# Performance work log

Hardware: AMD Instinct MI355X
Metric: run time of the kernel (lower is better)

The kernel has to match this reference:

```python
import jax, jax.numpy as jnp
import numpy as np

N = 100000   # atoms
E = 1600000  # edges (unused by this readout but required by signature)
C = 128      # channel multiplicity of node_feats irreps 128x0e+128x1o
PATH_W = 1.0 / 16.0  # e3nn uvu path weight: sqrt(1/(mul2_path0 + mul2_path1)) = sqrt(1/256)
SQRT3 = float(np.sqrt(3.0))


def setup_inputs() -> dict:
    key = jax.random.key(0)
    ks = jax.random.split(key, 32)
    r = lambda k, s, sc=1.0: jax.random.normal(k, s, dtype=jnp.float32) * sc
    z = lambda s: jnp.zeros(s, dtype=jnp.float32)
    return {
        # forward args
        "node_attrs": r(ks[0], (N, 10)),
        "node_feats": r(ks[1], (N, 4 * C)),           # 128x0e (128) + 128x1o (384)
        "edge_attrs": r(ks[2], (E, 9)),
        "edge_feats": r(ks[3], (E, 8)),
        "edge_index": jax.random.randint(ks[4], (2, E), 0, N),
        "field_feats": r(ks[5], (N, 4)),               # 1x0e + 1x1o
        "charges_0": r(ks[6], (N, 1)),
        "charges_induced": r(ks[7], (N, 1)),
        # o3.Linear(charges_irreps -> node_feats_irreps), fan_in=1 -> plain weight
        "Wq0": r(ks[8], (1, C)), "bq": z((C,)),
        # o3.Linear(potential_irreps -> node_feats_irreps)
        "Wv0": r(ks[9], (1, C)), "bv": z((C,)),
        "Wv1": r(ks[10], (1, C)),                      # 1o -> 128x1o path (no bias)
        # SparseUvuTensorProduct weights: path0 (0e x 0e -> 0e), path1 (1o x 1o -> 0e)
        "wq_s": r(ks[11], (C, C)), "wq_v": r(ks[12], (C, C)),
        "wv_s": r(ks[13], (C, C)), "wv_v": r(ks[14], (C, C)),
        # readout MLP [256,128,128,128,1] with SiLU between layers
        "W1": r(ks[15], (2 * C, 128), 1.0 / np.sqrt(2 * C)), "b1": z((128,)),
        "W2": r(ks[16], (128, 128), 1.0 / np.sqrt(128)), "b2": z((128,)),
        "W3": r(ks[17], (128, 128), 1.0 / np.sqrt(128)), "b3": z((128,)),
        "W4": r(ks[18], (128, 1), 1.0 / np.sqrt(128)), "b4": z((1,)),
    }


def _sparse_uvu_tp(x1s, x1v, x2s, x2v, w_s, w_v):
    """uvu TP (128x0e+128x1o) x (128x0e+128x1o) -> 128x0e, both paths to i_out=0.
    x1s/x2s: [N,C], x1v/x2v: [N,C,3]. Avoids the [N,C,C] pair matrix by
    contracting the weight into x2 first."""
    # path 0e x 0e -> 0e (d=1): mixed_bu = x1_bu * sum_v x2_bv w_uv
    out = x1s * (x2s @ w_s.T)
    # path 1o x 1o -> 0e (d=3): mixed_bu = sum_{v,d} x1_bud x2_bvd w_uv / sqrt(3)
    t = jnp.einsum('bvd,uv->bud', x2v, w_v)
    out = out + jnp.sum(x1v * t, axis=-1) / SQRT3
    return PATH_W * out


def reference(node_attrs, node_feats, edge_attrs, edge_feats, edge_index,
              field_feats, charges_0, charges_induced,
              Wq0, bq, Wv0, bv, Wv1,
              wq_s, wq_v, wv_s, wv_v,
              W1, b1, W2, b2, W3, b3, W4, b4):
    n = node_feats.shape[0]
    node_s = node_feats[:, :C]                 # [N,128] scalar block
    node_v = node_feats[:, C:].reshape(n, C, 3)  # [N,128,3] vector block (mul_ir)

    # q branch: linear_up_q(charges_induced + charges_0)
    q_in = charges_induced + charges_0         # [N,1]
    q_up_s = q_in @ Wq0 + bq                   # [N,128]
    q_up_v = jnp.zeros((n, C, 3), node_feats.dtype)  # 1x0e has no path to 128x1o

    # v branch: linear_up_v(field_feats)
    v_up_s = field_feats[:, :1] @ Wv0 + bv                     # [N,128]
    v_up_v = field_feats[:, None, 1:4] * Wv1[0][None, :, None]  # [N,128,3]

    dot_q = _sparse_uvu_tp(node_s, node_v, q_up_s, q_up_v, wq_s, wq_v)  # [N,128]
    dot_v = _sparse_uvu_tp(node_s, node_v, v_up_s, v_up_v, wv_s, wv_v)  # [N,128]

    h = jnp.concatenate([dot_q, dot_v], axis=-1)  # [N,256]
    h = jax.nn.silu(h @ W1 + b1)
    h = jax.nn.silu(h @ W2 + b2)
    h = jax.nn.silu(h @ W3 + b3)
    return h @ W4 + b4                           # [N,1] per-atom energy readout
```

## Files before the change

kernel.cpp:

```cpp
#include <hip/hip_runtime.h>
#include <hip/hip_bf16.h>

typedef __attribute__((ext_vector_type(8))) short short8;
typedef __attribute__((ext_vector_type(4))) float f32x4;

#define PATH_W 0.0625f
#define INV_SQRT3 0.57735026918962576f

typedef const __attribute__((address_space(1))) char gchar;
typedef __attribute__((address_space(3))) char schar;

__device__ __forceinline__ unsigned short f2bf(float f) {
    unsigned int u = __builtin_bit_cast(unsigned int, f);
    u += 0x7FFFu + ((u >> 16) & 1u);
    return (unsigned short)(u >> 16);
}

__device__ __forceinline__ float silu(float x) {
    return x / (1.0f + __expf(-x));
}

__global__ void prep_all(const float* __restrict__ Wq0, const float* __restrict__ bq,
                         const float* __restrict__ Wv0, const float* __restrict__ bv,
                         const float* __restrict__ Wv1, const float* __restrict__ wq_s,
                         const float* __restrict__ wv_s, const float* __restrict__ wv_v,
                         const float* __restrict__ W1, const float* __restrict__ W2,
                         const float* __restrict__ W3, const float* __restrict__ b1,
                         const float* __restrict__ b2, const float* __restrict__ b3,
                         const float* __restrict__ W4, const float* __restrict__ b4,
                         float* __restrict__ vecs, unsigned short* __restrict__ wp) {
    if (blockIdx.x == 0) {
        int u = threadIdx.x;
        float aq = 0.f, bqs = 0.f, av = 0.f, bvs = 0.f, a1 = 0.f;
        for (int v = 0; v < 128; ++v) {
            float rq = wq_s[u * 128 + v];
            float rv = wv_s[u * 128 + v];
            aq  += Wq0[v] * rq;
            bqs += bq[v]  * rq;
            av  += Wv0[v] * rv;
            bvs += bv[v]  * rv;
            a1  += Wv1[v] * wv_v[u * 128 + v];
        }
        vecs[u]        = PATH_W * aq;
        vecs[128 + u]  = PATH_W * bqs;
        vecs[256 + u]  = PATH_W * av;
        vecs[384 + u]  = PATH_W * bvs;
        vecs[512 + u]  = PATH_W * INV_SQRT3 * a1;
        vecs[640 + u]  = b1[u];
        vecs[768 + u]  = b2[u];
        vecs[896 + u]  = b3[u];
        vecs[1024 + u] = W4[u];
        if (u == 0) { vecs[1152] = b4[0]; vecs[1153] = 0.f; vecs[1154] = 0.f; vecs[1155] = 0.f; }
        return;
    }
    int fid  = blockIdx.x - 1;
    int t    = threadIdx.x;
    int lane = t & 63;
    int half = t >> 6;
    int g  = lane >> 4;
    int r  = lane & 15;
    const float* W;
    int row0, col;
    if (fid < 64) {
        int mt = fid >> 3, ks = fid & 7;
        W = W1; col = mt * 16 + r;
        row0 = ks * 32 + g * 8 + half * 4;
    } else {
        int f2 = fid < 96 ? fid - 64 : fid - 96;
        int mt = f2 >> 2, ks = f2 & 3;
        W = fid < 96 ? W2 : W3; col = mt * 16 + r;
        row0 = half * 64 + ks * 16 + g * 4;
    }
    unsigned short* dst = wp + fid * 512 + lane * 8 + half * 4;
    #pragma unroll
    for (int j = 0; j < 4; ++j) dst[j] = f2bf(W[(row0 + j) * 128 + col]);
}

__global__ __launch_bounds__(512, 1) void fused_main(
    const float* __restrict__ nf,
    const float* __restrict__ field,
    const float* __restrict__ c0, const float* __restrict__ ci,
    const float* __restrict__ vecs,
    const unsigned short* __restrict__ wp,
    float* __restrict__ out, int N)
{
    __shared__ __align__(16) char smem[131072];
    __shared__ __align__(16) float vlds[1156];
    const int tid  = threadIdx.x;
    const int wave = tid >> 6;
    const int lane = tid & 63;
    const int g    = lane >> 4;
    const int nl   = lane & 15;
    const int T    = (N + 127) >> 7;
    const char* wpb = (const char*)wp;

    #pragma unroll
    for (int i = 0; i < 16; ++i) {
        int off = (wave * 16 + i) * 1024;
        __builtin_amdgcn_global_load_lds((gchar*)(wpb + off + lane * 16),
                                         (schar*)(smem + off), 16, 0, 0);
    }
    if (wave == 0) {
        #pragma unroll
        for (int i = 0; i < 5; ++i) {
            int idx = lane + 64 * i;
            if (idx < 289)
                reinterpret_cast<f32x4*>(vlds)[idx] =
                    reinterpret_cast<const f32x4*>(vecs)[idx];
        }
    }

    f32x4 hs[4], hv0[4], hv1[4], hv2[4];
    float c0r, cir; f32x4 ffr;
    const char* bsr; const char* bvr;

#define SLOT_LOAD(sl_, q_, h_, bs_, bv_) {                                    \
        hs[sl_]  = *reinterpret_cast<const f32x4*>((bs_) + 128 * (q_) + 16 * (h_)); \
        hv0[sl_] = *reinterpret_cast<const f32x4*>((bv_) + 384 * (q_) + 48 * (h_)); \
        hv1[sl_] = *reinterpret_cast<const f32x4*>((bv_) + 384 * (q_) + 48 * (h_) + 16); \
        hv2[sl_] = *reinterpret_cast<const f32x4*>((bv_) + 384 * (q_) + 48 * (h_) + 32); }

    int tile = blockIdx.x;
    {
        int nd0 = tile * 128 + wave * 16 + nl;
        int ndc = nd0 < N ? nd0 : N - 1;
        const char* nrow = (const char*)nf + (size_t)ndc * 2048;
        bsr = nrow + 32 * g;
        bvr = nrow + 512 + 96 * g;
        #pragma unroll
        for (int qh = 0; qh < 2; ++qh)
            #pragma unroll
            for (int h = 0; h < 2; ++h)
                SLOT_LOAD(2 * qh + h, qh, h, bsr, bvr)
        c0r = c0[ndc]; cir = ci[ndc];
        ffr = reinterpret_cast<const f32x4*>(field)[ndc];
    }

    __syncthreads();

    const f32x4* vl4 = reinterpret_cast<const f32x4*>(vlds);

    for (; tile < T; tile += gridDim.x) {
        const int nd = tile * 128 + wave * 16 + nl;
        const int nt = tile + gridDim.x;
        const bool hasnext = nt < T;

        const char* bsn = bsr; const char* bvn = bvr;
        float c0n = 0.f, cin = 0.f; f32x4 ffn = ffr;
        if (hasnext) {
            int ndn = nt * 128 + wave * 16 + nl;
            ndn = ndn < N ? ndn : N - 1;
            const char* nrow = (const char*)nf + (size_t)ndn * 2048;
            bsn = nrow + 32 * g;
            bvn = nrow + 512 + 96 * g;
            c0n = c0[ndn]; cin = ci[ndn];
            ffn = reinterpret_cast<const f32x4*>(field)[ndn];
        }

        const float q_in = c0r + cir;
        const f32x4 ff   = ffr;

        f32x4 acc[8];
        #pragma unroll
        for (int mt = 0; mt < 8; ++mt) acc[mt] = vl4[160 + mt * 4 + g];

        short8 hfA, hfB;
        #pragma unroll
        for (int half = 0; half < 2; ++half) {
            #pragma unroll
            for (int qh = 0; qh < 2; ++qh) {
                const int q = 2 * half + qh;
                #pragma unroll
                for (int h = 0; h < 2; ++h) {
                    const int slot = 2 * qh + h;
                    const int m = 8 * q + 2 * g + h;
                    f32x4 aq = vl4[m], bqv = vl4[32 + m], av = vl4[64 + m],
                          bvv = vl4[96 + m], a1 = vl4[128 + m];
                    f32x4 s = hs[slot], va = hv0[slot], vb = hv1[slot], vc = hv2[slot];
                    float d3[4];
                    d3[0] = fmaf(va[0], ff[1], fmaf(va[1], ff[2], va[2] * ff[3]));
                    d3[1] = fmaf(va[3], ff[1], fmaf(vb[0], ff[2], vb[1] * ff[3]));
                    d3[2] = fmaf(vb[2], ff[1], fmaf(vb[3], ff[2], vc[0] * ff[3]));
                    d3[3] = fmaf(vc[1], ff[1], fmaf(vc[2], ff[2], vc[3] * ff[3]));
                    #pragma unroll
                    for (int j = 0; j < 4; ++j) {
                        float hq = s[j] * fmaf(q_in, aq[j], bqv[j]);
                        float hv = fmaf(s[j], fmaf(ff[0], av[j], bvv[j]), a1[j] * d3[j]);
                        if (h == 0) { hfA[j]     = (short)f2bf(hq); hfB[j]     = (short)f2bf(hv); }
                        else        { hfA[4 + j] = (short)f2bf(hq); hfB[4 + j] = (short)f2bf(hv); }
                    }
                    __builtin_amdgcn_sched_barrier(0);
                    if (half == 0) {
                        SLOT_LOAD(slot, qh + 2, h, bsr, bvr)
                    } else if (hasnext) {
                        SLOT_LOAD(slot, qh, h, bsn, bvn)
                    }
                }
                #pragma unroll
                for (int mt = 0; mt < 8; ++mt) {
                    short8 a0 = *reinterpret_cast<const short8*>(
                        smem + (mt * 8 + q) * 1024 + lane * 16);
                    acc[mt] = __builtin_amdgcn_mfma_f32_16x16x32_bf16(a0, hfA, acc[mt], 0, 0, 0);
                    short8 a4 = *reinterpret_cast<const short8*>(
                        smem + (mt * 8 + q + 4) * 1024 + lane * 16);
                    acc[mt] = __builtin_amdgcn_mfma_f32_16x16x32_bf16(a4, hfB, acc[mt], 0, 0, 0);
                }
            }
        }

        short8 hf2[4];
        #pragma unroll
        for (int ks = 0; ks < 4; ++ks)
            #pragma unroll
            for (int hp = 0; hp < 2; ++hp)
                #pragma unroll
                for (int j = 0; j < 4; ++j)
                    hf2[ks][hp * 4 + j] = (short)f2bf(silu(acc[hp * 4 + ks][j]));

        f32x4 acc2[8];
        #pragma unroll
        for (int mt = 0; mt < 8; ++mt) acc2[mt] = vl4[192 + mt * 4 + g];
        #pragma unroll
        for (int ks = 0; ks < 4; ++ks) {
            #pragma unroll
            for (int mt = 0; mt < 8; ++mt) {
                short8 a = *reinterpret_cast<const short8*>(
                    smem + 65536 + (mt * 4 + ks) * 1024 + lane * 16);
                acc2[mt] = __builtin_amdgcn_mfma_f32_16x16x32_bf16(a, hf2[ks], acc2[mt], 0, 0, 0);
            }
        }

        short8 hf3[4];
        #pragma unroll
        for (int ks = 0; ks < 4; ++ks)
            #pragma unroll
            for (int hp = 0; hp < 2; ++hp)
                #pragma unroll
                for (int j = 0; j < 4; ++j)
                    hf3[ks][hp * 4 + j] = (short)f2bf(silu(acc2[hp * 4 + ks][j]));

        f32x4 acc3[8];
        #pragma unroll
        for (int mt = 0; mt < 8; ++mt) acc3[mt] = vl4[224 + mt * 4 + g];
        #pragma unroll
        for (int ks = 0; ks < 4; ++ks) {
            #pragma unroll
            for (int mt = 0; mt < 8; ++mt) {
                short8 a = *reinterpret_cast<const short8*>(
                    smem + 98304 + (mt * 4 + ks) * 1024 + lane * 16);
                acc3[mt] = __builtin_amdgcn_mfma_f32_16x16x32_bf16(a, hf3[ks], acc3[mt], 0, 0, 0);
            }
        }

        float acc_out = 0.f;
        #pragma unroll
        for (int mt = 0; mt < 8; ++mt) {
            f32x4 w4v = vl4[256 + mt * 4 + g];
            acc_out += silu(acc3[mt][0]) * w4v[0];
            acc_out += silu(acc3[mt][1]) * w4v[1];
            acc_out += silu(acc3[mt][2]) * w4v[2];
            acc_out += silu(acc3[mt][3]) * w4v[3];
        }
        acc_out += __shfl_xor(acc_out, 16, 64);
        acc_out += __shfl_xor(acc_out, 32, 64);
        if (g == 0 && nd < N) out[nd] = acc_out + vlds[1152];

        bsr = bsn; bvr = bvn;
        c0r = c0n; cir = cin; ffr = ffn;
    }
#undef SLOT_LOAD
}

extern "C" void kernel_launch(void* const* d_in, const int* in_sizes, int n_in,
                              void* d_out, int out_size, void* d_ws, size_t ws_size,
                              hipStream_t stream) {
    const float* node_feats = (const float*)d_in[1];
    const float* field      = (const float*)d_in[5];
    const float* c0         = (const float*)d_in[6];
    const float* ci         = (const float*)d_in[7];
    const float* Wq0        = (const float*)d_in[8];
    const float* bq         = (const float*)d_in[9];
    const float* Wv0        = (const float*)d_in[10];
    const float* bv         = (const float*)d_in[11];
    const float* Wv1        = (const float*)d_in[12];
    const float* wq_s       = (const float*)d_in[13];
    const float* wv_s       = (const float*)d_in[15];
    const float* wv_v       = (const float*)d_in[16];
    const float* W1         = (const float*)d_in[17];
    const float* b1         = (const float*)d_in[18];
    const float* W2         = (const float*)d_in[19];
    const float* b2         = (const float*)d_in[20];
    const float* W3         = (const float*)d_in[21];
    const float* b3         = (const float*)d_in[22];
    const float* W4         = (const float*)d_in[23];
    const float* b4         = (const float*)d_in[24];

    const int N = in_sizes[1] / 512;
    float* vecs = (float*)d_ws;
    unsigned short* wp = (unsigned short*)((char*)d_ws + 8192);

    prep_all<<<129, 128, 0, stream>>>(Wq0, bq, Wv0, bv, Wv1, wq_s, wv_s, wv_v,
                                      W1, W2, W3, b1, b2, b3, W4, b4, vecs, wp);
    const int T = (N + 127) / 128;
    const int blocks = T < 256 ? T : 256;
    fused_main<<<blocks, 512, 0, stream>>>(node_feats, field, c0, ci, vecs, wp,
                                           (float*)d_out, N);
}
```

Before: 73.98 us.

## Run two 8-wave sub-blocks per 1024-thread block sharing LDS weights

Doubles the block to 1024 threads, split into two independent 8-wave groups that each stride over their own 128-node tiles, while the packed bf16 weights in LDS are loaded once and shared. The register prefetch of node features shrinks from four slots to a two-slot rolling buffer, and the launch bounds change to allow more waves per SIMD. The aim is more resident waves per CU to hide global-load latency in this memory-heavy readout. The tighter register budget risks spills, and each slot now has less prefetch lead time.

```diff
diff --git a/kernel.cpp b/kernel.cpp
--- a/kernel.cpp
+++ b/kernel.cpp
@@ -76,7 +76,7 @@
     for (int j = 0; j < 4; ++j) dst[j] = f2bf(W[(row0 + j) * 128 + col]);
 }
 
-__global__ __launch_bounds__(512, 1) void fused_main(
+__global__ __launch_bounds__(1024, 4) void fused_main(
     const float* __restrict__ nf,
     const float* __restrict__ field,
     const float* __restrict__ c0, const float* __restrict__ ci,
@@ -89,14 +89,17 @@
     const int tid  = threadIdx.x;
     const int wave = tid >> 6;
     const int lane = tid & 63;
+    const int sb   = wave >> 3;
+    const int w8   = wave & 7;
     const int g    = lane >> 4;
     const int nl   = lane & 15;
     const int T    = (N + 127) >> 7;
+    const int stride = gridDim.x * 2;
     const char* wpb = (const char*)wp;
 
     #pragma unroll
-    for (int i = 0; i < 16; ++i) {
-        int off = (wave * 16 + i) * 1024;
+    for (int i = 0; i < 8; ++i) {
+        int off = (wave * 8 + i) * 1024;
         __builtin_amdgcn_global_load_lds((gchar*)(wpb + off + lane * 16),
                                          (schar*)(smem + off), 16, 0, 0);
     }
@@ -110,7 +113,7 @@
         }
     }
 
-    f32x4 hs[4], hv0[4], hv1[4], hv2[4];
+    f32x4 hs[2], hv0[2], hv1[2], hv2[2];
     float c0r, cir; f32x4 ffr;
     const char* bsr; const char* bvr;
 
@@ -120,35 +123,32 @@
         hv1[sl_] = *reinterpret_cast<const f32x4*>((bv_) + 384 * (q_) + 48 * (h_) + 16); \
         hv2[sl_] = *reinterpret_cast<const f32x4*>((bv_) + 384 * (q_) + 48 * (h_) + 32); }
 
-    int tile = blockIdx.x;
+    int tile = blockIdx.x * 2 + sb;
     {
-        int nd0 = tile * 128 + wave * 16 + nl;
+        int nd0 = tile * 128 + w8 * 16 + nl;
         int ndc = nd0 < N ? nd0 : N - 1;
         const char* nrow = (const char*)nf + (size_t)ndc * 2048;
         bsr = nrow + 32 * g;
         bvr = nrow + 512 + 96 * g;
-        #pragma unroll
-        for (int qh = 0; qh < 2; ++qh)
-            #pragma unroll
-            for (int h = 0; h < 2; ++h)
-                SLOT_LOAD(2 * qh + h, qh, h, bsr, bvr)
         c0r = c0[ndc]; cir = ci[ndc];
         ffr = reinterpret_cast<const f32x4*>(field)[ndc];
+        SLOT_LOAD(0, 0, 0, bsr, bvr)
+        SLOT_LOAD(1, 0, 1, bsr, bvr)
     }
 
     __syncthreads();
 
     const f32x4* vl4 = reinterpret_cast<const f32x4*>(vlds);
 
-    for (; tile < T; tile += gridDim.x) {
-        const int nd = tile * 128 + wave * 16 + nl;
-        const int nt = tile + gridDim.x;
+    for (; tile < T; tile += stride) {
+        const int nd = tile * 128 + w8 * 16 + nl;
+        const int nt = tile + stride;
         const bool hasnext = nt < T;
 
         const char* bsn = bsr; const char* bvn = bvr;
         float c0n = 0.f, cin = 0.f; f32x4 ffn = ffr;
         if (hasnext) {
-            int ndn = nt * 128 + wave * 16 + nl;
+            int ndn = nt * 128 + w8 * 16 + nl;
             ndn = ndn < N ? ndn : N - 1;
             const char* nrow = (const char*)nf + (size_t)ndn * 2048;
             bsn = nrow + 32 * g;
@@ -166,45 +166,43 @@
 
         short8 hfA, hfB;
         #pragma unroll
-        for (int half = 0; half < 2; ++half) {
-            #pragma unroll
-            for (int qh = 0; qh < 2; ++qh) {
-                const int q = 2 * half + qh;
+        for (int q = 0; q < 4; ++q) {
+            #pragma unroll
+            for (int h = 0; h < 2; ++h) {
+                const int p = 2 * q + h;
+                const int slot = p & 1;
+                const int m = 8 * q + 2 * g + h;
+                f32x4 aq = vl4[m], bqv = vl4[32 + m], av = vl4[64 + m],
+                      bvv = vl4[96 + m], a1 = vl4[128 + m];
+                f32x4 s = hs[slot], va = hv0[slot], vb = hv1[slot], vc = hv2[slot];
+                float d3[4];
+                d3[0] = fmaf(va[0], ff[1], fmaf(va[1], ff[2], va[2] * ff[3]));
+                d3[1] = fmaf(va[3], ff[1], fmaf(vb[0], ff[2], vb[1] * ff[3]));
+                d3[2] = fmaf(vb[2], ff[1], fmaf(vb[3], ff[2], vc[0] * ff[3]));
+                d3[3] = fmaf(vc[1], ff[1], fmaf(vc[2], ff[2], vc[3] * ff[3]));
                 #pragma unroll
-                for (int h = 0; h < 2; ++h) {
-                    const int slot = 2 * qh + h;
-                    const int m = 8 * q + 2 * g + h;
-                    f32x4 aq = vl4[m], bqv = vl4[32 + m], av = vl4[64 + m],
-                          bvv = vl4[96 + m], a1 = vl4[128 + m];
-                    f32x4 s = hs[slot], va = hv0[slot], vb = hv1[slot], vc = hv2[slot];
-                    float d3[4];
-                    d3[0] = fmaf(va[0], ff[1], fmaf(va[1], ff[2], va[2] * ff[3]));
-                    d3[1] = fmaf(va[3], ff[1], fmaf(vb[0], ff[2], vb[1] * ff[3]));
-                    d3[2] = fmaf(vb[2], ff[1], fmaf(vb[3], ff[2], vc[0] * ff[3]));
-                    d3[3] = fmaf(vc[1], ff[1], fmaf(vc[2], ff[2], vc[3] * ff[3]));
-                    #pragma unroll
-                    for (int j = 0; j < 4; ++j) {
-                        float hq = s[j] * fmaf(q_in, aq[j], bqv[j]);
-                        float hv = fmaf(s[j], fmaf(ff[0], av[j], bvv[j]), a1[j] * d3[j]);
-                        if (h == 0) { hfA[j]     = (short)f2bf(hq); hfB[j]     = (short)f2bf(hv); }
-                        else        { hfA[4 + j] = (short)f2bf(hq); hfB[4 + j] = (short)f2bf(hv); }
-                    }
-                    __builtin_amdgcn_sched_barrier(0);
-                    if (half == 0) {
-                        SLOT_LOAD(slot, qh + 2, h, bsr, bvr)
-                    } else if (hasnext) {
-                        SLOT_LOAD(slot, qh, h, bsn, bvn)
-                    }
+                for (int j = 0; j < 4; ++j) {
+                    float hq = s[j] * fmaf(q_in, aq[j], bqv[j]);
+                    float hv = fmaf(s[j], fmaf(ff[0], av[j], bvv[j]), a1[j] * d3[j]);
+                    if (h == 0) { hfA[j]     = (short)f2bf(hq); hfB[j]     = (short)f2bf(hv); }
+                    else        { hfA[4 + j] = (short)f2bf(hq); hfB[4 + j] = (short)f2bf(hv); }
                 }
-                #pragma unroll
-                for (int mt = 0; mt < 8; ++mt) {
-                    short8 a0 = *reinterpret_cast<const short8*>(
-                        smem + (mt * 8 + q) * 1024 + lane * 16);
-                    acc[mt] = __builtin_amdgcn_mfma_f32_16x16x32_bf16(a0, hfA, acc[mt], 0, 0, 0);
-                    short8 a4 = *reinterpret_cast<const short8*>(
-                        smem + (mt * 8 + q + 4) * 1024 + lane * 16);
-                    acc[mt] = __builtin_amdgcn_mfma_f32_16x16x32_bf16(a4, hfB, acc[mt], 0, 0, 0);
+                __builtin_amdgcn_sched_barrier(0);
+                if (p < 6) {
+                    const int pn = p + 2;
+                    SLOT_LOAD(slot, pn >> 1, pn & 1, bsr, bvr)
+                } else if (hasnext) {
+                    SLOT_LOAD(slot, 0, p - 6, bsn, bvn)
                 }
+            }
+            #pragma unroll
+            for (int mt = 0; mt < 8; ++mt) {
+                short8 a0 = *reinterpret_cast<const short8*>(
+                    smem + (mt * 8 + q) * 1024 + lane * 16);
+                acc[mt] = __builtin_amdgcn_mfma_f32_16x16x32_bf16(a0, hfA, acc[mt], 0, 0, 0);
+                short8 a4 = *reinterpret_cast<const short8*>(
+                    smem + (mt * 8 + q + 4) * 1024 + lane * 16);
+                acc[mt] = __builtin_amdgcn_mfma_f32_16x16x32_bf16(a4, hfB, acc[mt], 0, 0, 0);
             }
         }
 
@@ -302,7 +300,8 @@
     prep_all<<<129, 128, 0, stream>>>(Wq0, bq, Wv0, bv, Wv1, wq_s, wv_s, wv_v,
                                       W1, W2, W3, b1, b2, b3, W4, b4, vecs, wp);
     const int T = (N + 127) / 128;
-    const int blocks = T < 256 ? T : 256;
-    fused_main<<<blocks, 512, 0, stream>>>(node_feats, field, c0, ci, vecs, wp,
-                                           (float*)d_out, N);
-}
+    int blocks = (T + 1) / 2;
+    if (blocks > 256) blocks = 256;
+    fused_main<<<blocks, 1024, 0, stream>>>(node_feats, field, c0, ci, vecs, wp,
+                                            (float*)d_out, N);
+}
```

New measurement: 96.80 us. 1.31x slower.
